# Performance work log

Hardware: AMD Instinct MI355X
Metric: run time of the kernel (lower is better)

Reference implementation:

```python
import jax, jax.numpy as jnp
import numpy as np

D = 768      # d_model (BERT-base)
H = 8        # MatTransformer heads
DK = D // H  # 96
L = 4        # MatTransformer layers
FF = 1024    # MatTransformer hidden_size
NREL = 97    # num_relations
BAG = 8      # bag_len (docs per bag)
SEQ = 512    # seq_len
NB = 3       # bridge entities per doc
S = 2 + NB   # spans per doc: h, t, bridges
E = BAG * S  # total entities = 40
NEG = -1e30


def setup_inputs() -> dict:
    key = jax.random.key(0)
    ks = jax.random.split(key, 30)
    w = lambda k, shp: jax.random.normal(k, shp, jnp.float32) * 0.02
    inp = {
        "embedding": jax.random.normal(ks[0], (BAG, SEQ, D), jnp.float32),
        "spans": jnp.sort(jax.random.randint(ks[1], (BAG, S, 2), 0, SEQ, jnp.int32), axis=-1),
        # Codred pairwise-relation params (torch Linear stored as [in, out])
        "wu_w": w(ks[2], (D, D)), "wu_b": jnp.zeros((D,), jnp.float32),
        "wvv_w": w(ks[3], (D, D)), "wvv_b": jnp.zeros((D,), jnp.float32),
        "lnr_w": w(ks[4], (D, D)), "lnr_b": jnp.zeros((D,), jnp.float32),
        # MatTransformer params, stacked over layers
        "matt_wq": w(ks[5], (L, D, D)), "matt_bq": jnp.zeros((L, D), jnp.float32),
        "matt_wk": w(ks[6], (L, D, D)), "matt_bk": jnp.zeros((L, D), jnp.float32),
        "matt_wv": w(ks[7], (L, D, D)), "matt_bv": jnp.zeros((L, D), jnp.float32),
        "matt_wo": w(ks[8], (L, D, D)), "matt_bo": jnp.zeros((L, D), jnp.float32),
        "matt_w1": w(ks[9], (L, D, FF)), "matt_b1": jnp.zeros((L, FF), jnp.float32),
        "matt_w2": w(ks[10], (L, FF, D)), "matt_b2": jnp.zeros((L, D), jnp.float32),
        "matt_g1": jnp.ones((L, D), jnp.float32), "matt_be1": jnp.zeros((L, D), jnp.float32),
        "matt_g2": jnp.ones((L, D), jnp.float32), "matt_be2": jnp.zeros((L, D), jnp.float32),
        # relation predictor
        "pred_w": w(ks[11], (D, NREL)), "pred_b": jnp.zeros((NREL,), jnp.float32),
    }
    return inp


def _layernorm(x, g, b, eps=1e-5):
    m = jnp.mean(x, axis=-1, keepdims=True)
    v = jnp.var(x, axis=-1, keepdims=True)
    return (x - m) * jax.lax.rsqrt(v + eps) * g + b


def reference(embedding, spans, wu_w, wu_b, wvv_w, wvv_b, lnr_w, lnr_b,
              matt_wq, matt_bq, matt_wk, matt_bk, matt_wv, matt_bv, matt_wo, matt_bo,
              matt_w1, matt_b1, matt_w2, matt_b2, matt_g1, matt_be1, matt_g2, matt_be2,
              pred_w, pred_b):
    # --- entity span max-pool (gather + max over inclusive [start, end]) ---
    pos = jnp.arange(SEQ)
    span_mask = (pos[None, None, :] >= spans[..., 0:1]) & (pos[None, None, :] <= spans[..., 1:2])  # [BAG,S,SEQ]
    pooled = jnp.max(jnp.where(span_mask[..., None], embedding[:, None, :, :], NEG), axis=2)  # [BAG,S,D]
    htb = pooled.reshape(E, D)  # per-doc order: h, t, b1..bNB (matches htb_embs stacking)

    # --- pairwise relation matrix: relu(ln1(relu(u_i + v_j))) ---
    u = htb @ wu_w + wu_b                       # [E,D]
    v = htb @ wvv_w + wvv_b                     # [E,D]
    alpha = jax.nn.relu(u[:, None, :] + v[None, :, :])          # [E,E,D]
    rel = jax.nn.relu(alpha @ lnr_w + lnr_b)                    # [E,E,D]

    # --- MatTransformer: encoder over the E*E relation tokens (rel_mask all ones) ---
    T = E * E
    x = rel.reshape(T, D)
    scale = 1.0 / np.sqrt(DK).astype(np.float32)
    for l in range(L):
        q = (x @ matt_wq[l] + matt_bq[l]).reshape(T, H, DK)
        k = (x @ matt_wk[l] + matt_bk[l]).reshape(T, H, DK)
        vv = (x @ matt_wv[l] + matt_bv[l]).reshape(T, H, DK)
        scores = jnp.einsum('thd,shd->hts', q, k) * scale       # [H,T,T]
        attn = jax.nn.softmax(scores, axis=-1)
        o = jnp.einsum('hts,shd->thd', attn, vv).reshape(T, D)
        o = o @ matt_wo[l] + matt_bo[l]
        x = _layernorm(x + o, matt_g1[l], matt_be1[l])
        ff = jax.nn.relu(x @ matt_w1[l] + matt_b1[l]) @ matt_w2[l] + matt_b2[l]
        x = _layernorm(x + ff, matt_g2[l], matt_be2[l])
    rel_m = x.reshape(E, E, D)

    # --- gather (h, t) relation features, predict, bag max-pool over logits ---
    h_pos = jnp.arange(BAG) * S      # head entity index per doc
    t_pos = h_pos + 1                # tail entity index per doc
    ht_feat = rel_m[h_pos, t_pos]    # [BAG,D]
    ht_logits = ht_feat @ pred_w + pred_b          # [BAG,NREL]
    bag_logit = jnp.max(ht_logits, axis=0, keepdims=True)  # [1,NREL]
    return bag_logit
```

## Files before the change

### kernel.cpp

```cpp
#include <hip/hip_runtime.h>


#define D    768
#define H    8
#define DKD  96
#define LAY  4
#define FFD  1024
#define NREL 97
#define BAG  8
#define SPANS 5
#define E    40
#define TT   1600
#define SEQ  512
#define D3   2304
#define NS   3

typedef __attribute__((ext_vector_type(8))) short bf16x8;
typedef __attribute__((ext_vector_type(4))) float f32x4;
typedef unsigned short ushort_t;
typedef unsigned int uint_t;

__device__ __forceinline__ ushort_t f2b(float x) {
    uint_t u = __builtin_bit_cast(uint_t, x);
    return (ushort_t)((u + 0x7fffu + ((u >> 16) & 1u)) >> 16);
}
__device__ __forceinline__ float b2f(ushort_t v) {
    return __builtin_bit_cast(float, (uint_t)v << 16);
}

__device__ __forceinline__ void gload16(const void* g, void* l) {
    __builtin_amdgcn_global_load_lds(
        (const __attribute__((address_space(1))) unsigned int*)g,
        (__attribute__((address_space(3))) unsigned int*)l, 16, 0, 0);
}

__device__ __forceinline__ float block_sum(float v, float* red) {
#pragma unroll
    for (int o = 32; o >= 1; o >>= 1) v += __shfl_xor(v, o);
    __syncthreads();
    if ((threadIdx.x & 63) == 0) red[threadIdx.x >> 6] = v;
    __syncthreads();
    return red[0] + red[1] + red[2] + red[3];
}

__global__ __launch_bounds__(256) void span_pool_p1(const float* __restrict__ emb,
        const int* __restrict__ spans, float* __restrict__ partial) {
    const int e = blockIdx.x, pg = blockIdx.y;
    const int bag = e / SPANS;
    const int st = spans[e * 2 + 0];
    const int en = spans[e * 2 + 1];
    const int p0 = max(st, pg * 64);
    const int p1 = min(en, pg * 64 + 63);
    const int tid = threadIdx.x;
    if (tid >= 192) return;
    float4 m = make_float4(-1e30f, -1e30f, -1e30f, -1e30f);
    for (int p = p0; p <= p1; ++p) {
        const float4 v = *(const float4*)(emb + ((size_t)bag * SEQ + p) * D + tid * 4);
        m.x = fmaxf(m.x, v.x); m.y = fmaxf(m.y, v.y);
        m.z = fmaxf(m.z, v.z); m.w = fmaxf(m.w, v.w);
    }
    *(float4*)(partial + ((size_t)e * 8 + pg) * D + tid * 4) = m;
}

__global__ __launch_bounds__(256) void span_pool_p2(const float* __restrict__ partial,
        ushort_t* __restrict__ htb) {
    const int e = blockIdx.x;
    const int tid = threadIdx.x;
    if (tid >= 192) return;
    float4 m = make_float4(-1e30f, -1e30f, -1e30f, -1e30f);
#pragma unroll
    for (int pg = 0; pg < 8; ++pg) {
        const float4 v = *(const float4*)(partial + ((size_t)e * 8 + pg) * D + tid * 4);
        m.x = fmaxf(m.x, v.x); m.y = fmaxf(m.y, v.y);
        m.z = fmaxf(m.z, v.z); m.w = fmaxf(m.w, v.w);
    }
    ushort4 o;
    o.x = f2b(m.x); o.y = f2b(m.y); o.z = f2b(m.z); o.w = f2b(m.w);
    *(ushort4*)(htb + (size_t)e * D + tid * 4) = o;
}

__global__ __launch_bounds__(256) void alpha_k(const float* __restrict__ uv,
        ushort_t* __restrict__ a) {
    const int ij = blockIdx.x;
    const int i = ij / E, j = ij % E;
    const int tid = threadIdx.x;
#pragma unroll
    for (int t2 = 0; t2 < 3; ++t2) {
        const int d = tid + t2 * 256;
        a[(size_t)ij * D + d] =
            f2b(fmaxf(uv[(size_t)i * 1536 + d] + uv[(size_t)j * 1536 + 768 + d], 0.f));
    }
}

__global__ __launch_bounds__(256) void transpose_up(const float* __restrict__ lnr,
        const float* __restrict__ wu, const float* __restrict__ wvv,
        ushort_t* __restrict__ lnrT, ushort_t* __restrict__ wuvT) {
    __shared__ float t[32][33];
    const int z = blockIdx.z;
    const float* src = (z == 0) ? lnr : (z == 1) ? wu : wvv;
    ushort_t* dst = (z == 0) ? lnrT : wuvT + (size_t)(z - 1) * D * D;
    const int n0 = blockIdx.x * 32, k0 = blockIdx.y * 32;
    const int tx = threadIdx.x & 31, ty = threadIdx.x >> 5;
#pragma unroll
    for (int i = 0; i < 4; ++i)
        t[ty + i * 8][tx] = src[(size_t)(k0 + ty + i * 8) * D + n0 + tx];
    __syncthreads();
#pragma unroll
    for (int i = 0; i < 4; ++i)
        dst[(size_t)(n0 + ty + i * 8) * D + k0 + tx] = f2b(t[tx][ty + i * 8]);
}

__global__ __launch_bounds__(256) void transpose_layer(const float* __restrict__ wq,
        const float* __restrict__ wk, const float* __restrict__ wv,
        const float* __restrict__ wo, const float* __restrict__ w1,
        const float* __restrict__ w2, int l, ushort_t* __restrict__ wT4,
        ushort_t* __restrict__ w1T, ushort_t* __restrict__ w2T) {
    __shared__ float t[32][33];
    const int z = blockIdx.z;
    const float* src; ushort_t* dst; int K, N;
    if (z < 4) {
        K = D; N = D;
        src = (z == 0 ? wq : z == 1 ? wk : z == 2 ? wv : wo) + (size_t)l * D * D;
        dst = wT4 + (size_t)z * D * D;
    } else if (z == 4) {
        K = D; N = FFD; src = w1 + (size_t)l * D * FFD; dst = w1T;
    } else {
        K = FFD; N = D; src = w2 + (size_t)l * FFD * D; dst = w2T;
    }
    const int n0 = blockIdx.x * 32, k0 = blockIdx.y * 32;
    if (n0 >= N || k0 >= K) return;
    const int tx = threadIdx.x & 31, ty = threadIdx.x >> 5;
#pragma unroll
    for (int i = 0; i < 4; ++i)
        t[ty + i * 8][tx] = src[(size_t)(k0 + ty + i * 8) * N + n0 + tx];
    __syncthreads();
#pragma unroll
    for (int i = 0; i < 4; ++i)
        dst[(size_t)(n0 + ty + i * 8) * K + k0 + tx] = f2b(t[tx][ty + i * 8]);
}

__global__ __launch_bounds__(256) void concat_bias(const float* __restrict__ bq,
        const float* __restrict__ bk, const float* __restrict__ bv,
        const float* __restrict__ bu, const float* __restrict__ bvv,
        float* __restrict__ bqkv, float* __restrict__ buv) {
    const int i = blockIdx.x * 256 + threadIdx.x;
    if (i < LAY * D3) {
        const int l = i / D3, j = i % D3;
        bqkv[i] = j < D ? bq[l * D + j] : j < 2 * D ? bk[l * D + j - D] : bv[l * D + j - 2 * D];
    }
    const int k = i - LAY * D3;
    if (k >= 0 && k < 2 * D) buv[k] = k < D ? bu[k] : bvv[k - D];
}

template<int RELU, int SCALEQ, int SPLITK>
__global__ __launch_bounds__(256) void gemm_mfma(const ushort_t* __restrict__ A,
        const ushort_t* __restrict__ Bt, const float* __restrict__ bias,
        float* __restrict__ Cf, float* __restrict__ Cf1,
        ushort_t* __restrict__ Cb, int M, int N, int K) {
    __shared__ ushort_t As[2][128 * 32];
    __shared__ ushort_t Bs[2][64 * 32];
    const int tid = threadIdx.x;
    const int lane = tid & 63, w = tid >> 6;
    const int l15 = lane & 15, lg = lane >> 4;
    const int bm = blockIdx.y * 128, bn = blockIdx.x * 64;
    const int wm = (w >> 1) * 64, wn = (w & 1) * 32;
    const int trA0 = w * 32 + (lane >> 2);
    const int trA1 = trA0 + 16;
    const int trB  = w * 16 + (lane >> 2);
    const int sc   = (lane & 3) * 8;
    const size_t rowA0 = (size_t)min(bm + trA0, M - 1) * K;
    const size_t rowA1 = (size_t)min(bm + trA1, M - 1) * K;
    const size_t rowB  = (size_t)(bn + trB) * K;
    const int kbeg = SPLITK ? blockIdx.z * (K / 2) : 0;
    const int kend = SPLITK ? kbeg + K / 2 : K;

    f32x4 acc[4][2];
#pragma unroll
    for (int mi = 0; mi < 4; ++mi)
#pragma unroll
        for (int ni = 0; ni < 2; ++ni)
            acc[mi][ni] = (f32x4){0.f, 0.f, 0.f, 0.f};

    auto STAGE = [&](int buf, int k0) {
        gload16(A + rowA0 + k0 + sc, As[buf] + w * 1024);
        gload16(A + rowA1 + k0 + sc, As[buf] + w * 1024 + 512);
        gload16(Bt + rowB + k0 + sc, Bs[buf] + w * 512);
    };

    const int ntk = (kend - kbeg) / 32;
    STAGE(0, kbeg);
    __syncthreads();
    for (int t = 0; t < ntk; ++t) {
        const int buf = t & 1;
        if (t + 1 < ntk) STAGE(buf ^ 1, kbeg + (t + 1) * 32);
        bf16x8 af[4], bfr[2];
#pragma unroll
        for (int mi = 0; mi < 4; ++mi)
            af[mi] = *(const bf16x8*)&As[buf][(wm + mi * 16 + l15) * 32 + lg * 8];
#pragma unroll
        for (int ni = 0; ni < 2; ++ni)
            bfr[ni] = *(const bf16x8*)&Bs[buf][(wn + ni * 16 + l15) * 32 + lg * 8];
        __builtin_amdgcn_s_setprio(1);
#pragma unroll
        for (int mi = 0; mi < 4; ++mi)
#pragma unroll
            for (int ni = 0; ni < 2; ++ni)
                acc[mi][ni] = __builtin_amdgcn_mfma_f32_16x16x32_bf16(
                    af[mi], bfr[ni], acc[mi][ni], 0, 0, 0);
        __builtin_amdgcn_s_setprio(0);
        __syncthreads();
    }
    float* Cout = (SPLITK && blockIdx.z) ? Cf1 : Cf;
    const bool addb = !(SPLITK && blockIdx.z);
#pragma unroll
    for (int mi = 0; mi < 4; ++mi)
#pragma unroll
        for (int ni = 0; ni < 2; ++ni)
#pragma unroll
            for (int r = 0; r < 4; ++r) {
                const int row = bm + wm + mi * 16 + lg * 4 + r;
                if (row >= M) continue;
                const int col = bn + wn + ni * 16 + l15;
                float v = acc[mi][ni][r] + (addb ? bias[col] : 0.f);
                if (RELU) v = fmaxf(v, 0.f);
                if (SCALEQ) { if (col < D) v *= 0.10206207261596577f; }
                if (Cout) Cout[(size_t)row * N + col] = v;
                if (Cb) Cb[(size_t)row * N + col] = f2b(v);
            }
}

__global__ __launch_bounds__(256) void attn_part(const ushort_t* __restrict__ qkv,
        ushort_t* __restrict__ Opart, float* __restrict__ ml) {
    __shared__ ushort_t Ks[64][104];
    __shared__ ushort_t Vt[96][72];
    __shared__ ushort_t Ps[4][16][72];
    const int q0 = blockIdx.x * 64;
    const int h = blockIdx.y;
    const int cch = blockIdx.z;
    const int t_lo = (cch * (TT / 64)) / NS;
    const int t_hi = ((cch + 1) * (TT / 64)) / NS;
    const int tid = threadIdx.x;
    const int lane = tid & 63, w = tid >> 6;
    const int l15 = lane & 15, lg = lane >> 4;

    int r_[3], c_[3];
#pragma unroll
    for (int i = 0; i < 3; ++i) {
        const int ch = i * 256 + tid;
        r_[i] = ch / 12; c_[i] = (ch % 12) * 8;
    }
    bf16x8 qfrag[3];
#pragma unroll
    for (int ks = 0; ks < 3; ++ks)
        qfrag[ks] = *(const bf16x8*)(qkv + (size_t)(q0 + w * 16 + l15) * D3
                                     + h * DKD + ks * 32 + lg * 8);
    uint4 kreg[3], vreg[3];
    {
        const int s0 = t_lo * 64;
#pragma unroll
        for (int i = 0; i < 3; ++i) {
            kreg[i] = *(const uint4*)(qkv + (size_t)(s0 + r_[i]) * D3 + D + h * DKD + c_[i]);
            vreg[i] = *(const uint4*)(qkv + (size_t)(s0 + r_[i]) * D3 + 2 * D + h * DKD + c_[i]);
        }
    }
    float m_run[4], l_run[4];
    f32x4 acc_o[6];
#pragma unroll
    for (int r = 0; r < 4; ++r) { m_run[r] = -1e30f; l_run[r] = 0.f; }
#pragma unroll
    for (int nt = 0; nt < 6; ++nt) acc_o[nt] = (f32x4){0.f, 0.f, 0.f, 0.f};

    for (int t = t_lo; t < t_hi; ++t) {
        __syncthreads();
#pragma unroll
        for (int i = 0; i < 3; ++i) {
            *(uint4*)&Ks[r_[i]][c_[i]] = kreg[i];
            const ushort_t* pv = (const ushort_t*)&vreg[i];
            const int kk = r_[i] ^ (((c_[i] >> 3) & 7) << 3);
#pragma unroll
            for (int j = 0; j < 8; ++j) Vt[c_[i] + j][kk] = pv[j];
        }
        __syncthreads();
        if (t + 1 < t_hi) {
            const int s0 = (t + 1) * 64;
#pragma unroll
            for (int i = 0; i < 3; ++i) {
                kreg[i] = *(const uint4*)(qkv + (size_t)(s0 + r_[i]) * D3 + D + h * DKD + c_[i]);
                vreg[i] = *(const uint4*)(qkv + (size_t)(s0 + r_[i]) * D3 + 2 * D + h * DKD + c_[i]);
            }
        }
        f32x4 accs[4];
#pragma unroll
        for (int ni = 0; ni < 4; ++ni) accs[ni] = (f32x4){0.f, 0.f, 0.f, 0.f};
        __builtin_amdgcn_s_setprio(1);
#pragma unroll
        for (int ks = 0; ks < 3; ++ks) {
#pragma unroll
            for (int ni = 0; ni < 4; ++ni) {
                const bf16x8 bk = *(const bf16x8*)&Ks[ni * 16 + l15][ks * 32 + lg * 8];
                accs[ni] = __builtin_amdgcn_mfma_f32_16x16x32_bf16(qfrag[ks], bk, accs[ni], 0, 0, 0);
            }
        }
        __builtin_amdgcn_s_setprio(0);
        float mx[4];
#pragma unroll
        for (int r = 0; r < 4; ++r) {
            mx[r] = fmaxf(fmaxf(accs[0][r], accs[1][r]), fmaxf(accs[2][r], accs[3][r]));
#pragma unroll
            for (int o = 1; o <= 8; o <<= 1) mx[r] = fmaxf(mx[r], __shfl_xor(mx[r], o));
        }
        const bool grow = (mx[0] > m_run[0] + 8.f) || (mx[1] > m_run[1] + 8.f) ||
                          (mx[2] > m_run[2] + 8.f) || (mx[3] > m_run[3] + 8.f);
        if (__any(grow)) {
#pragma unroll
            for (int r = 0; r < 4; ++r) {
                const float mnew = fmaxf(m_run[r], mx[r]);
                const float sf = __expf(m_run[r] - mnew);
                m_run[r] = mnew;
                l_run[r] *= sf;
#pragma unroll
                for (int nt = 0; nt < 6; ++nt) acc_o[nt][r] *= sf;
            }
        }
        float ps[4][4];
#pragma unroll
        for (int r = 0; r < 4; ++r) {
            float rs = 0.f;
#pragma unroll
            for (int ni = 0; ni < 4; ++ni) {
                ps[ni][r] = __expf(accs[ni][r] - m_run[r]);
                rs += ps[ni][r];
            }
#pragma unroll
            for (int o = 1; o <= 8; o <<= 1) rs += __shfl_xor(rs, o);
            l_run[r] += rs;
        }
#pragma unroll
        for (int ni = 0; ni < 4; ++ni)
#pragma unroll
            for (int r = 0; r < 4; ++r)
                Ps[w][lg * 4 + r][ni * 16 + l15] = f2b(ps[ni][r]);
        __builtin_amdgcn_s_setprio(1);
#pragma unroll
        for (int ks = 0; ks < 2; ++ks) {
            const bf16x8 ap = *(const bf16x8*)&Ps[w][l15][ks * 32 + lg * 8];
#pragma unroll
            for (int nt = 0; nt < 6; ++nt) {
                const int dim = nt * 16 + l15;
                const int kcol = (ks * 32 + lg * 8) ^ (((dim >> 3) & 7) << 3);
                const bf16x8 bv = *(const bf16x8*)&Vt[dim][kcol];
                acc_o[nt] = __builtin_amdgcn_mfma_f32_16x16x32_bf16(ap, bv, acc_o[nt], 0, 0, 0);
            }
        }
        __builtin_amdgcn_s_setprio(0);
    }
    __syncthreads();
    ushort_t* scr = &Ks[0][0] + w * (16 * 104);
#pragma unroll
    for (int nt = 0; nt < 6; ++nt)
#pragma unroll
        for (int r = 0; r < 4; ++r)
            scr[(lg * 4 + r) * 104 + nt * 16 + l15] = f2b(acc_o[nt][r]);
    const size_t obase = (((size_t)cch * H + h) * TT + q0 + w * 16) * DKD;
#pragma unroll
    for (int ch = 0; ch < 3; ++ch) {
        const int idx = ch * 64 + lane;
        const int row = idx / 12;
        const int c16 = (idx % 12) * 8;
        const uint4 v = *(const uint4*)&scr[row * 104 + c16];
        *(uint4*)(Opart + obase + (size_t)row * DKD + c16) = v;
    }
    if (l15 == 0) {
#pragma unroll
        for (int r = 0; r < 4; ++r) {
            const int row = q0 + w * 16 + lg * 4 + r;
            float2* mlp = (float2*)ml;
            mlp[((size_t)cch * H + h) * TT + row] = make_float2(m_run[r], l_run[r]);
        }
    }
}

__global__ __launch_bounds__(256) void attn_combine(const ushort_t* __restrict__ Opart,
        const float* __restrict__ ml, ushort_t* __restrict__ O) {
    const int row = blockIdx.x;
    const int tid = threadIdx.x;
    const float2* mlp = (const float2*)ml;
#pragma unroll
    for (int kk = 0; kk < 3; ++kk) {
        const int col = tid + kk * 256;
        const int h = col / DKD, d = col % DKD;
        float m[NS], l[NS], M = -1e30f;
#pragma unroll
        for (int c = 0; c < NS; ++c) {
            const float2 v = mlp[((size_t)c * H + h) * TT + row];
            m[c] = v.x; l[c] = v.y; M = fmaxf(M, m[c]);
        }
        float L = 0.f, o = 0.f;
#pragma unroll
        for (int c = 0; c < NS; ++c) {
            const float e = __expf(m[c] - M);
            L += l[c] * e;
            o += b2f(Opart[(((size_t)c * H + h) * TT + row) * DKD + d]) * e;
        }
        O[(size_t)row * D + col] = f2b(o / L);
    }
}

__global__ __launch_bounds__(256) void add_ln3(float* __restrict__ x,
        const float* __restrict__ y0, const float* __restrict__ y1,
        const float* __restrict__ g, const float* __restrict__ b,
        ushort_t* __restrict__ xb) {
    const int lane = threadIdx.x & 63, w = threadIdx.x >> 6;
    const int row = blockIdx.x * 4 + w;
    const size_t base = (size_t)row * D;
    float4 t[3];
    float s = 0.f, s2 = 0.f;
#pragma unroll
    for (int i = 0; i < 3; ++i) {
        const int c = lane * 4 + i * 256;
        const float4 xv = *(const float4*)(x + base + c);
        const float4 a0 = *(const float4*)(y0 + base + c);
        const float4 a1 = *(const float4*)(y1 + base + c);
        t[i].x = xv.x + a0.x + a1.x; t[i].y = xv.y + a0.y + a1.y;
        t[i].z = xv.z + a0.z + a1.z; t[i].w = xv.w + a0.w + a1.w;
        s += t[i].x + t[i].y + t[i].z + t[i].w;
        s2 += t[i].x * t[i].x + t[i].y * t[i].y + t[i].z * t[i].z + t[i].w * t[i].w;
    }
#pragma unroll
    for (int o = 32; o >= 1; o >>= 1) { s += __shfl_xor(s, o); s2 += __shfl_xor(s2, o); }
    const float mean = s * (1.f / 768.f);
    const float var = s2 * (1.f / 768.f) - mean * mean;
    const float inv = rsqrtf(var + 1e-5f);
#pragma unroll
    for (int i = 0; i < 3; ++i) {
        const int c = lane * 4 + i * 256;
        float4 o4;
        o4.x = (t[i].x - mean) * inv * g[c + 0] + b[c + 0];
        o4.y = (t[i].y - mean) * inv * g[c + 1] + b[c + 1];
        o4.z = (t[i].z - mean) * inv * g[c + 2] + b[c + 2];
        o4.w = (t[i].w - mean) * inv * g[c + 3] + b[c + 3];
        *(float4*)(x + base + c) = o4;
        ushort4 u;
        u.x = f2b(o4.x); u.y = f2b(o4.y); u.z = f2b(o4.z); u.w = f2b(o4.w);
        *(ushort4*)(xb + base + c) = u;
    }
}

__global__ __launch_bounds__(256) void predict_k(const float* __restrict__ x,
        const float* __restrict__ pw, const float* __restrict__ pb,
        float* __restrict__ out) {
    __shared__ float red[4];
    const int r = blockIdx.x;
    const int tid = threadIdx.x;
    float best = -1e30f;
    for (int bag = 0; bag < BAG; ++bag) {
        const int row = (bag * SPANS) * E + (bag * SPANS + 1);
        const float* f = x + (size_t)row * D;
        float acc = 0.f;
        for (int d = tid; d < D; d += 256) acc += f[d] * pw[(size_t)d * NREL + r];
        best = fmaxf(best, block_sum(acc, red));
    }
    if (tid == 0) out[r] = best + pb[r];
}

extern "C" void kernel_launch(void* const* d_in, const int* in_sizes, int n_in,
                              void* d_out, int out_size, void* d_ws, size_t ws_size,
                              hipStream_t stream) {
    const float* emb  = (const float*)d_in[0];
    const int*  spans = (const int*)d_in[1];
    const float* wu_w = (const float*)d_in[2];  const float* wu_b = (const float*)d_in[3];
    const float* wvv_w= (const float*)d_in[4];  const float* wvv_b= (const float*)d_in[5];
    const float* lnr_w= (const float*)d_in[6];  const float* lnr_b= (const float*)d_in[7];
    const float* wq = (const float*)d_in[8];    const float* bq = (const float*)d_in[9];
    const float* wk = (const float*)d_in[10];   const float* bk = (const float*)d_in[11];
    const float* wv = (const float*)d_in[12];   const float* bv = (const float*)d_in[13];
    const float* wo = (const float*)d_in[14];   const float* bo = (const float*)d_in[15];
    const float* w1 = (const float*)d_in[16];   const float* b1 = (const float*)d_in[17];
    const float* w2 = (const float*)d_in[18];   const float* b2 = (const float*)d_in[19];
    const float* g1 = (const float*)d_in[20];   const float* be1= (const float*)d_in[21];
    const float* g2 = (const float*)d_in[22];   const float* be2= (const float*)d_in[23];
    const float* pw = (const float*)d_in[24];   const float* pb = (const float*)d_in[25];

    char* cur = (char*)d_ws;
    auto alloc = [&](size_t bytes) { char* p = cur; cur += (bytes + 255) & ~(size_t)255; return p; };
    ushort_t* htb  = (ushort_t*)alloc(E * D * 2);
    float*    uvb  = (float*)alloc((size_t)E * 1536 * 4);
    float*    part = (float*)alloc((size_t)E * 8 * D * 4);
    float*    x    = (float*)alloc((size_t)TT * D * 4);
    ushort_t* xb   = (ushort_t*)alloc((size_t)TT * D * 2);
    ushort_t* qkv  = (ushort_t*)alloc((size_t)TT * D3 * 2);
    ushort_t* ob   = (ushort_t*)alloc((size_t)TT * D * 2);
    float*    tb   = (float*)alloc((size_t)TT * D * 4);
    ushort_t* fb   = (ushort_t*)alloc((size_t)TT * FFD * 2);
    ushort_t* wT4  = (ushort_t*)alloc((size_t)4 * D * D * 2);
    ushort_t* w1T  = (ushort_t*)alloc((size_t)D * FFD * 2);
    ushort_t* w2T  = (ushort_t*)alloc((size_t)FFD * D * 2);
    float*    bqkv = (float*)alloc((size_t)LAY * D3 * 4);
    float*    buv  = (float*)alloc((size_t)2 * D * 4);
    ushort_t* Opart = (ushort_t*)tb;
    float*    ml    = part;
    ushort_t* wuvT  = wT4;
    ushort_t* lnrT  = w1T;
    float*    tb1   = (float*)qkv;

    const int DD = D * D;

    span_pool_p1<<<dim3(E, 8), 256, 0, stream>>>(emb, spans, part);
    span_pool_p2<<<E, 256, 0, stream>>>(part, htb);
    transpose_up<<<dim3(24, 24, 3), 256, 0, stream>>>(lnr_w, wu_w, wvv_w, lnrT, wuvT);
    concat_bias<<<(LAY * D3 + 2 * D + 255) / 256, 256, 0, stream>>>(bq, bk, bv, wu_b, wvv_b, bqkv, buv);
    gemm_mfma<0, 0, 0><<<dim3(1536 / 64, 1), 256, 0, stream>>>(
        htb, wuvT, buv, uvb, nullptr, nullptr, E, 1536, D);
    alpha_k<<<TT, 256, 0, stream>>>(uvb, ob);
    gemm_mfma<1, 0, 0><<<dim3(D / 64, (TT + 127) / 128), 256, 0, stream>>>(
        ob, lnrT, lnr_b, x, nullptr, xb, TT, D, D);

    for (int l = 0; l < LAY; ++l) {
        transpose_layer<<<dim3(32, 32, 6), 256, 0, stream>>>(wq, wk, wv, wo, w1, w2, l, wT4, w1T, w2T);
        gemm_mfma<0, 1, 0><<<dim3(D3 / 64, (TT + 127) / 128), 256, 0, stream>>>(
            xb, wT4, bqkv + l * D3, nullptr, nullptr, qkv, TT, D3, D);
        attn_part<<<dim3(TT / 64, H, NS), 256, 0, stream>>>(qkv, Opart, ml);
        attn_combine<<<TT, 256, 0, stream>>>(Opart, ml, ob);
        gemm_mfma<0, 0, 1><<<dim3(D / 64, (TT + 127) / 128, 2), 256, 0, stream>>>(
            ob, wT4 + 3 * DD, bo + l * D, tb, tb1, nullptr, TT, D, D);
        add_ln3<<<TT / 4, 256, 0, stream>>>(x, tb, tb1, g1 + l * D, be1 + l * D, xb);
        gemm_mfma<1, 0, 0><<<dim3(FFD / 64, (TT + 127) / 128), 256, 0, stream>>>(
            xb, w1T, b1 + l * FFD, nullptr, nullptr, fb, TT, FFD, D);
        gemm_mfma<0, 0, 1><<<dim3(D / 64, (TT + 127) / 128, 2), 256, 0, stream>>>(
            fb, w2T, b2 + l * D, tb, tb1, nullptr, TT, D, FFD);
        add_ln3<<<TT / 4, 256, 0, stream>>>(x, tb, tb1, g2 + l * D, be2 + l * D, xb);
    }

    predict_k<<<NREL, 256, 0, stream>>>(x, pw, pb, (float*)d_out);
    (void)in_sizes; (void)n_in; (void)out_size; (void)ws_size;
}
```

Baseline: 599.9 us.

## Prefetch K/V two tiles ahead in attention and remap block indices

The attention-partial kernel now keeps two register sets for K/V tiles and issues global loads two iterations ahead, with the loop manually unrolled by two, so more memory latency is hidden behind the MFMA work. The launch grid is flattened to 1D with the head index in the low bits, so blocks sharing the same key/value chunk and query tile but different heads are scheduled next to each other. The deeper prefetch costs extra VGPRs, which can lower occupancy.

```diff
diff --git a/kernel.cpp b/kernel.cpp
--- a/kernel.cpp
+++ b/kernel.cpp
@@ -14,6 +14,7 @@
 #define SEQ  512
 #define D3   2304
 #define NS   3
+#define QT   (TT / 64)
 
 typedef __attribute__((ext_vector_type(8))) short bf16x8;
 typedef __attribute__((ext_vector_type(4))) float f32x4;
@@ -234,11 +235,14 @@
     __shared__ ushort_t Ks[64][104];
     __shared__ ushort_t Vt[96][72];
     __shared__ ushort_t Ps[4][16][72];
-    const int q0 = blockIdx.x * 64;
-    const int h = blockIdx.y;
-    const int cch = blockIdx.z;
-    const int t_lo = (cch * (TT / 64)) / NS;
-    const int t_hi = ((cch + 1) * (TT / 64)) / NS;
+    const int bid = blockIdx.x;
+    const int h   = bid & 7;
+    const int t7  = bid >> 3;
+    const int cch = t7 / QT;
+    const int qt  = t7 % QT;
+    const int q0 = qt * 64;
+    const int t_lo = (cch * QT) / NS;
+    const int t_hi = ((cch + 1) * QT) / NS;
     const int tid = threadIdx.x;
     const int lane = tid & 63, w = tid >> 6;
     const int l15 = lane & 15, lg = lane >> 4;
@@ -254,15 +258,16 @@
     for (int ks = 0; ks < 3; ++ks)
         qfrag[ks] = *(const bf16x8*)(qkv + (size_t)(q0 + w * 16 + l15) * D3
                                      + h * DKD + ks * 32 + lg * 8);
-    uint4 kreg[3], vreg[3];
-    {
-        const int s0 = t_lo * 64;
+
+    auto LOADT = [&](int t, uint4 (&kr)[3], uint4 (&vr)[3]) {
+        const int s0 = t * 64;
 #pragma unroll
         for (int i = 0; i < 3; ++i) {
-            kreg[i] = *(const uint4*)(qkv + (size_t)(s0 + r_[i]) * D3 + D + h * DKD + c_[i]);
-            vreg[i] = *(const uint4*)(qkv + (size_t)(s0 + r_[i]) * D3 + 2 * D + h * DKD + c_[i]);
-        }
-    }
+            kr[i] = *(const uint4*)(qkv + (size_t)(s0 + r_[i]) * D3 + D + h * DKD + c_[i]);
+            vr[i] = *(const uint4*)(qkv + (size_t)(s0 + r_[i]) * D3 + 2 * D + h * DKD + c_[i]);
+        }
+    };
+
     float m_run[4], l_run[4];
     f32x4 acc_o[6];
 #pragma unroll
@@ -270,25 +275,19 @@
 #pragma unroll
     for (int nt = 0; nt < 6; ++nt) acc_o[nt] = (f32x4){0.f, 0.f, 0.f, 0.f};
 
-    for (int t = t_lo; t < t_hi; ++t) {
+    auto BODY = [&](int t, uint4 (&kr)[3], uint4 (&vr)[3],
+                    uint4 (&krn)[3], uint4 (&vrn)[3]) {
         __syncthreads();
 #pragma unroll
         for (int i = 0; i < 3; ++i) {
-            *(uint4*)&Ks[r_[i]][c_[i]] = kreg[i];
-            const ushort_t* pv = (const ushort_t*)&vreg[i];
+            *(uint4*)&Ks[r_[i]][c_[i]] = kr[i];
+            const ushort_t* pv = (const ushort_t*)&vr[i];
             const int kk = r_[i] ^ (((c_[i] >> 3) & 7) << 3);
 #pragma unroll
             for (int j = 0; j < 8; ++j) Vt[c_[i] + j][kk] = pv[j];
         }
         __syncthreads();
-        if (t + 1 < t_hi) {
-            const int s0 = (t + 1) * 64;
-#pragma unroll
-            for (int i = 0; i < 3; ++i) {
-                kreg[i] = *(const uint4*)(qkv + (size_t)(s0 + r_[i]) * D3 + D + h * DKD + c_[i]);
-                vreg[i] = *(const uint4*)(qkv + (size_t)(s0 + r_[i]) * D3 + 2 * D + h * DKD + c_[i]);
-            }
-        }
+        if (t + 2 < t_hi) LOADT(t + 2, krn, vrn);
         f32x4 accs[4];
 #pragma unroll
         for (int ni = 0; ni < 4; ++ni) accs[ni] = (f32x4){0.f, 0.f, 0.f, 0.f};
@@ -353,7 +352,16 @@
             }
         }
         __builtin_amdgcn_s_setprio(0);
-    }
+    };
+
+    uint4 krA[3], vrA[3], krB[3], vrB[3];
+    LOADT(t_lo, krA, vrA);
+    if (t_lo + 1 < t_hi) LOADT(t_lo + 1, krB, vrB);
+    for (int t = t_lo; t < t_hi; t += 2) {
+        BODY(t, krA, vrA, krA, vrA);
+        if (t + 1 < t_hi) BODY(t + 1, krB, vrB, krB, vrB);
+    }
+
     __syncthreads();
     ushort_t* scr = &Ks[0][0] + w * (16 * 104);
 #pragma unroll
@@ -519,7 +527,7 @@
         transpose_layer<<<dim3(32, 32, 6), 256, 0, stream>>>(wq, wk, wv, wo, w1, w2, l, wT4, w1T, w2T);
         gemm_mfma<0, 1, 0><<<dim3(D3 / 64, (TT + 127) / 128), 256, 0, stream>>>(
             xb, wT4, bqkv + l * D3, nullptr, nullptr, qkv, TT, D3, D);
-        attn_part<<<dim3(TT / 64, H, NS), 256, 0, stream>>>(qkv, Opart, ml);
+        attn_part<<<H * NS * QT, 256, 0, stream>>>(qkv, Opart, ml);
         attn_combine<<<TT, 256, 0, stream>>>(Opart, ml, ob);
         gemm_mfma<0, 0, 1><<<dim3(D / 64, (TT + 127) / 128, 2), 256, 0, stream>>>(
             ob, wT4 + 3 * DD, bo + l * D, tb, tb1, nullptr, TT, D, D);
```

New measurement: 633.2 us. +5.5%, slower.
